# Kernel optimization log

Measured on AMD Instinct MI355X. Metric: run time of the kernel, lower is better.

Reference implementation:

```python
import jax, jax.numpy as jnp
import numpy as np
import math

N_EMBD = 1024
N_HEADS = 16
B, T = 4, 2048

def setup_inputs() -> dict:
    key = jax.random.key(0)
    k1, k2, k3 = jax.random.split(key, 3)
    x = jax.random.normal(k1, (B, T, N_EMBD), dtype=jnp.float32)
    scale = 1.0 / math.sqrt(N_EMBD)
    W_attn = jax.random.normal(k2, (N_EMBD, 3 * N_EMBD), dtype=jnp.float32) * scale
    W_proj = jax.random.normal(k3, (N_EMBD, N_EMBD), dtype=jnp.float32) * scale
    return {"x": x, "W_attn": W_attn, "W_proj": W_proj}

def reference(x, W_attn, W_proj):
    Bb, Tt, C = x.shape
    hd = C // N_HEADS
    qkv = x @ W_attn  # [B,T,3C]
    q, k, v = jnp.split(qkv, 3, axis=-1)
    # [B,H,T,hd]
    q = q.reshape(Bb, Tt, N_HEADS, hd).transpose(0, 2, 1, 3)
    k = k.reshape(Bb, Tt, N_HEADS, hd).transpose(0, 2, 1, 3)
    v = v.reshape(Bb, Tt, N_HEADS, hd).transpose(0, 2, 1, 3)
    att = jnp.einsum('bhqd,bhkd->bhqk', q, k) * (1.0 / math.sqrt(hd))
    mask = jnp.tril(jnp.ones((Tt, Tt), dtype=bool))
    att = jnp.where(mask[None, None], att, -jnp.inf)
    att = jax.nn.softmax(att, axis=-1)
    out = jnp.einsum('bhqk,bhkd->bhqd', att, v)
    out = out.transpose(0, 2, 1, 3).reshape(Bb, Tt, C)
    return out @ W_proj
```

## Files before the change

kernel.cpp:

```cpp
#include <hip/hip_runtime.h>
#include <cstddef>
#include <cstdint>

typedef __attribute__((ext_vector_type(8))) _Float16 half8;
typedef __attribute__((ext_vector_type(4))) _Float16 half4;
typedef __attribute__((ext_vector_type(4))) float f32x4;
typedef __attribute__((ext_vector_type(16))) float f32x16;

#define N_EMBD 1024
#define N_HEADS 16
#define BATCH 4
#define SEQ 2048
#define C3 3072
#define HD 64

__device__ inline uint32_t pk2(float x, float y) {
    auto h2 = __builtin_amdgcn_cvt_pkrtz(x, y);
    uint32_t u;
    __builtin_memcpy(&u, &h2, 4);
    return u;
}

__device__ inline void swap32(uint32_t& a, uint32_t& b) {
    asm volatile("v_permlane32_swap_b32 %0, %1" : "+v"(a), "+v"(b));
}

__device__ inline float exp2_hw(float x) {
    float r;
    asm("v_exp_f32 %0, %1" : "=v"(r) : "v"(x));
    return r;
}

__global__ void cvt_f32_f16(const float* __restrict__ in, _Float16* __restrict__ out, int n) {
    int i = (blockIdx.x * 256 + threadIdx.x) * 4;
    if (i >= n) return;
    float4 v = *(const float4*)(in + i);
    half4 h;
    h[0] = (_Float16)v.x; h[1] = (_Float16)v.y; h[2] = (_Float16)v.z; h[3] = (_Float16)v.w;
    *(half4*)(out + i) = h;
}

__global__ void transpose_cvt(const float* __restrict__ in, _Float16* __restrict__ out,
                              int R, int Ncols) {
    __shared__ float tile[32][33];
    int n0 = blockIdx.x * 32, r0 = blockIdx.y * 32;
    int tx = threadIdx.x, ty = threadIdx.y;
#pragma unroll
    for (int i = 0; i < 32; i += 8)
        tile[ty + i][tx] = in[(size_t)(r0 + ty + i) * Ncols + n0 + tx];
    __syncthreads();
#pragma unroll
    for (int i = 0; i < 32; i += 8)
        out[(size_t)(n0 + ty + i) * R + r0 + tx] = (_Float16)tile[tx][ty + i];
}

__global__ void transpose_v(const _Float16* __restrict__ qkv, _Float16* __restrict__ vT) {
    __shared__ _Float16 tile[32][36];
    int t0 = blockIdx.x * 32;
    int bhd = blockIdx.y;
    int bh = bhd >> 1, dh = bhd & 1;
    int b = bh >> 4, h = bh & 15;
    int tx = threadIdx.x, ty = threadIdx.y;
#pragma unroll
    for (int i = 0; i < 32; i += 8)
        tile[ty + i][tx] = qkv[(size_t)(b * SEQ + t0 + ty + i) * C3 + 2 * N_EMBD + h * HD + dh * 32 + tx];
    __syncthreads();
#pragma unroll
    for (int i = 0; i < 32; i += 8)
        vT[((size_t)bh * HD + dh * 32 + ty + i) * SEQ + t0 + tx] = tile[tx][ty + i];
}

__device__ inline void store1(float* p, float v) { *p = v; }
__device__ inline void store1(_Float16* p, float v) { *p = (_Float16)v; }

template <typename OutT>
__global__ __launch_bounds__(512, 1) void gemm192(
    const _Float16* __restrict__ A, const _Float16* __restrict__ Bt,
    OutT* __restrict__ C, int M, int N, int K) {
    __shared__ _Float16 Al[2][256 * 64];
    __shared__ _Float16 Bl[2][192 * 64];
    const int tid = threadIdx.x;
    const int lane = tid & 63, wave = tid >> 6;
    const int l15 = lane & 15, l4 = lane >> 4;
    const int wm = wave >> 2, wn = wave & 3;

    const int nwg = gridDim.x, nbx = N / 192;
    int wg = blockIdx.x;
    if ((nwg & 7) == 0) { int cpx = nwg >> 3; wg = (wg & 7) * cpx + (wg >> 3); }
    const int row0 = (wg / nbx) * 256, col0 = (wg % nbx) * 192;
    const int TAU = K >> 6;

    const int srow = tid >> 3, su = tid & 7;
    const int usrc8 = (su ^ (srow & 7)) * 8;
    auto stageAu = [&](int unit, int ts) {
        __builtin_amdgcn_global_load_lds(
            (const __attribute__((address_space(1))) void*)(A + (size_t)(row0 + unit * 64 + srow) * K + ts * 64 + usrc8),
            (__attribute__((address_space(3))) void*)(&Al[ts & 1][unit * 64 * 64 + tid * 8]), 16, 0, 0);
    };
    auto stageBu = [&](int unit, int ts) {
        __builtin_amdgcn_global_load_lds(
            (const __attribute__((address_space(1))) void*)(Bt + (size_t)(col0 + unit * 64 + srow) * K + ts * 64 + usrc8),
            (__attribute__((address_space(3))) void*)(&Bl[ts & 1][unit * 64 * 64 + tid * 8]), 16, 0, 0);
    };
    auto stageTile = [&](int ts) {
        stageAu(0, ts); stageAu(1, ts); stageAu(2, ts); stageAu(3, ts);
        stageBu(0, ts); stageBu(1, ts); stageBu(2, ts);
    };

    f32x4 acc[8][3] = {};
    stageTile(0); stageTile(1);
    asm volatile("s_waitcnt vmcnt(7)" ::: "memory");
    __builtin_amdgcn_s_barrier();

    half8 a[4][2], b[3][2];
    for (int tau = 0; tau < TAU; ++tau) {
        const _Float16* Ab = &Al[tau & 1][0];
        const _Float16* Bb = &Bl[tau & 1][0];
        const bool t2 = (tau + 2 < TAU);

#pragma unroll
        for (int m = 0; m < 4; ++m)
#pragma unroll
            for (int ks = 0; ks < 2; ++ks) {
                int r = wm * 128 + m * 16 + l15;
                a[m][ks] = *(const half8*)(Ab + r * 64 + (((ks * 4 + l4) ^ (r & 7)) * 8));
            }
#pragma unroll
        for (int n = 0; n < 3; ++n)
#pragma unroll
            for (int ks = 0; ks < 2; ++ks) {
                int r = wn * 48 + n * 16 + l15;
                b[n][ks] = *(const half8*)(Bb + r * 64 + (((ks * 4 + l4) ^ (r & 7)) * 8));
            }
        __builtin_amdgcn_s_barrier();
        __builtin_amdgcn_s_setprio(1);
#pragma unroll
        for (int m = 0; m < 4; ++m)
#pragma unroll
            for (int n = 0; n < 2; ++n)
#pragma unroll
                for (int ks = 0; ks < 2; ++ks)
                    acc[m][n] = __builtin_amdgcn_mfma_f32_16x16x32_f16(a[m][ks], b[n][ks], acc[m][n], 0, 0, 0);
        __builtin_amdgcn_s_setprio(0);
        __builtin_amdgcn_s_barrier();

        if (t2) { stageBu(0, tau + 2); stageBu(1, tau + 2); stageBu(2, tau + 2); }
        __builtin_amdgcn_s_barrier();
        __builtin_amdgcn_s_setprio(1);
#pragma unroll
        for (int m = 0; m < 4; ++m)
#pragma unroll
            for (int ks = 0; ks < 2; ++ks)
                acc[m][2] = __builtin_amdgcn_mfma_f32_16x16x32_f16(a[m][ks], b[2][ks], acc[m][2], 0, 0, 0);
        __builtin_amdgcn_s_setprio(0);
        __builtin_amdgcn_s_barrier();

#pragma unroll
        for (int m = 0; m < 4; ++m)
#pragma unroll
            for (int ks = 0; ks < 2; ++ks) {
                int r = wm * 128 + 64 + m * 16 + l15;
                a[m][ks] = *(const half8*)(Ab + r * 64 + (((ks * 4 + l4) ^ (r & 7)) * 8));
            }
        if (t2) { stageAu(0, tau + 2); stageAu(2, tau + 2); }
        __builtin_amdgcn_s_barrier();
        __builtin_amdgcn_s_setprio(1);
#pragma unroll
        for (int m = 0; m < 4; ++m)
#pragma unroll
            for (int n = 0; n < 2; ++n)
#pragma unroll
                for (int ks = 0; ks < 2; ++ks)
                    acc[4 + m][n] = __builtin_amdgcn_mfma_f32_16x16x32_f16(a[m][ks], b[n][ks], acc[4 + m][n], 0, 0, 0);
        __builtin_amdgcn_s_setprio(0);
        __builtin_amdgcn_s_barrier();

        if (t2) { stageAu(1, tau + 2); stageAu(3, tau + 2); }
        __builtin_amdgcn_s_barrier();
        __builtin_amdgcn_s_setprio(1);
#pragma unroll
        for (int m = 0; m < 4; ++m)
#pragma unroll
            for (int ks = 0; ks < 2; ++ks)
                acc[4 + m][2] = __builtin_amdgcn_mfma_f32_16x16x32_f16(a[m][ks], b[2][ks], acc[4 + m][2], 0, 0, 0);
        __builtin_amdgcn_s_setprio(0);
        if (tau <= TAU - 3) {
            asm volatile("s_waitcnt vmcnt(7)" ::: "memory");
        } else if (tau == TAU - 2) {
            asm volatile("s_waitcnt vmcnt(0)" ::: "memory");
        }
        __builtin_amdgcn_s_barrier();
    }

#pragma unroll
    for (int mi = 0; mi < 8; ++mi)
#pragma unroll
        for (int ni = 0; ni < 3; ++ni)
#pragma unroll
            for (int j = 0; j < 4; ++j) {
                int r = row0 + wm * 128 + (mi >> 2) * 64 + (mi & 3) * 16 + l4 * 4 + j;
                int c = col0 + wn * 48 + ni * 16 + l15;
                store1(C + (size_t)r * N + c, acc[mi][ni][j]);
            }
}

template <typename OutT>
__global__ __launch_bounds__(256, 2) void gemm_h(
    const _Float16* __restrict__ A, const _Float16* __restrict__ Bt,
    OutT* __restrict__ C, int M, int N, int K) {
    __shared__ _Float16 Al[128 * 32];
    __shared__ _Float16 Bl[128 * 32];
    const int tid = threadIdx.x;
    const int wave = tid >> 6, lane = tid & 63;
    const int l15 = lane & 15, l4 = lane >> 4;
    const int gx = gridDim.x;
    int lin = blockIdx.y * gx + blockIdx.x;
    int bcol, brow;
    if ((gx & 7) == 0) {
        int cpx = gx >> 3;
        int xcd = lin & 7;
        int idx = lin >> 3;
        bcol = xcd * cpx + idx % cpx;
        brow = idx / cpx;
    } else { bcol = blockIdx.x; brow = blockIdx.y; }
    const int row0 = brow * 128, col0 = bcol * 128;
    const int wm = wave >> 1, wn = wave & 1;
    f32x4 acc[4][4] = {};
    for (int k0 = 0; k0 < K; k0 += 32) {
#pragma unroll
        for (int i = 0; i < 2; ++i) {
            int c = tid + 256 * i;
            int r = c >> 2, c8 = (c & 3) * 8;
            __builtin_amdgcn_global_load_lds(
                (const __attribute__((address_space(1))) void*)(A + (size_t)(row0 + r) * K + k0 + c8),
                (__attribute__((address_space(3))) void*)(Al + (size_t)(wave * 64 + 256 * i) * 8),
                16, 0, 0);
        }
#pragma unroll
        for (int i = 0; i < 2; ++i) {
            int c = tid + 256 * i;
            int r = c >> 2, c8 = (c & 3) * 8;
            __builtin_amdgcn_global_load_lds(
                (const __attribute__((address_space(1))) void*)(Bt + (size_t)(col0 + r) * K + k0 + c8),
                (__attribute__((address_space(3))) void*)(Bl + (size_t)(wave * 64 + 256 * i) * 8),
                16, 0, 0);
        }
        __syncthreads();
        half8 a[4], b[4];
#pragma unroll
        for (int m = 0; m < 4; ++m)
            a[m] = *(const half8*)(Al + (wm * 64 + m * 16 + l15) * 32 + l4 * 8);
#pragma unroll
        for (int n = 0; n < 4; ++n)
            b[n] = *(const half8*)(Bl + (wn * 64 + n * 16 + l15) * 32 + l4 * 8);
        __builtin_amdgcn_s_setprio(1);
#pragma unroll
        for (int m = 0; m < 4; ++m)
#pragma unroll
            for (int n = 0; n < 4; ++n)
                acc[m][n] = __builtin_amdgcn_mfma_f32_16x16x32_f16(a[m], b[n], acc[m][n], 0, 0, 0);
        __builtin_amdgcn_s_setprio(0);
        __syncthreads();
    }
#pragma unroll
    for (int m = 0; m < 4; ++m)
#pragma unroll
        for (int n = 0; n < 4; ++n)
#pragma unroll
            for (int j = 0; j < 4; ++j) {
                int r = row0 + wm * 64 + m * 16 + l4 * 4 + j;
                int cc = col0 + wn * 64 + n * 16 + l15;
                store1(C + (size_t)r * N + cc, acc[m][n][j]);
            }
}

__global__ __launch_bounds__(256, 3) void attn_kernel(const _Float16* __restrict__ qkv,
                                                      const _Float16* __restrict__ vT,
                                                      _Float16* __restrict__ ao) {
    const int bid = blockIdx.x;
    const int pairp = bid >> 6;
    const int bh = bid & 63;
    const int b = bh >> 4, h = bh & 15;
    const int tid = threadIdx.x, lane = tid & 63;
    const int wave = tid >> 6;
    const int l31 = lane & 31, L = lane >> 5;

    __shared__ _Float16 Kl[3][64 * 64];
    __shared__ _Float16 Vl[3][64 * 64];

    const float qscale = 0.125f * 1.44269504089f;
    const float NEGC = -4.0f * 1.44269504089f;

    auto stage = [&](int t, int buf) {
#pragma unroll
        for (int i = 0; i < 2; ++i) {
            int idx = tid + 256 * i;
            int key = idx >> 3;
            int d8 = ((idx & 7) ^ (key & 7)) * 8;
            __builtin_amdgcn_global_load_lds(
                (const __attribute__((address_space(1))) void*)(qkv + (size_t)(b * SEQ + t * 64 + key) * C3 + N_EMBD + h * HD + d8),
                (__attribute__((address_space(3))) void*)(&Kl[buf][idx * 8]), 16, 0, 0);
        }
#pragma unroll
        for (int i = 0; i < 2; ++i) {
            int idx = tid + 256 * i;
            int d = idx >> 3;
            int k8 = ((idx & 7) ^ (d & 7)) * 8;
            __builtin_amdgcn_global_load_lds(
                (const __attribute__((address_space(1))) void*)(vT + ((size_t)bh * HD + d) * SEQ + t * 64 + k8),
                (__attribute__((address_space(3))) void*)(&Vl[buf][idx * 8]), 16, 0, 0);
        }
    };

    half8 onesf;
#pragma unroll
    for (int e = 0; e < 8; ++e) onesf[e] = (_Float16)1.0f;
    const f32x16 cinit = (f32x16)(NEGC);

    for (int pass = 0; pass < 2; ++pass) {
        const int qt = pass ? (15 - pairp) : pairp;
        const int q0w = qt * 128 + wave * 32;
        const int q_g = q0w + l31;
        const int nt = 2 * qt + 2;

        stage(0, 0);
        stage(1, 1);

        half8 qb[4];
#pragma unroll
        for (int ks = 0; ks < 4; ++ks) {
            half8 v = *(const half8*)(qkv + (size_t)(b * SEQ + q_g) * C3 + h * HD + ks * 16 + L * 8);
#pragma unroll
            for (int e = 0; e < 8; ++e) v[e] = (_Float16)((float)v[e] * qscale);
            qb[ks] = v;
        }

        f32x16 o[2];
        o[0] = (f32x16)(0.f);
        o[1] = (f32x16)(0.f);
        f32x16 lac = (f32x16)(0.f);

        asm volatile("s_waitcnt vmcnt(4)" ::: "memory");
        __builtin_amdgcn_s_barrier();

        int cur = 0;
        for (int t = 0; t < nt; ++t) {
            const int kv0 = t * 64;
            int sb = cur + 2; if (sb >= 3) sb -= 3;
            if (t + 2 < nt) stage(t + 2, sb);

            if (kv0 <= q0w + 31) {
                const _Float16* Kb = &Kl[cur][0];
                const _Float16* Vb = &Vl[cur][0];
                f32x16 s[2];
                __builtin_amdgcn_s_setprio(1);
#pragma unroll
                for (int kb = 0; kb < 2; ++kb) {
                    const int key = kb * 32 + l31;
                    {
                        half8 kf = *(const half8*)(Kb + key * 64 + ((L ^ (key & 7)) * 8));
                        s[kb] = __builtin_amdgcn_mfma_f32_32x32x16_f16(kf, qb[0], cinit, 0, 0, 0);
                    }
#pragma unroll
                    for (int ks = 1; ks < 4; ++ks) {
                        half8 kf = *(const half8*)(Kb + key * 64 + (((ks * 2 + L) ^ (key & 7)) * 8));
                        s[kb] = __builtin_amdgcn_mfma_f32_32x32x16_f16(kf, qb[ks], s[kb], 0, 0, 0);
                    }
                }
                __builtin_amdgcn_s_setprio(0);
                const bool needmask = (kv0 + 63 > q0w);
#pragma unroll
                for (int kb = 0; kb < 2; ++kb) {
#pragma unroll
                    for (int r = 0; r < 16; ++r) {
                        float v = exp2_hw(s[kb][r]);
                        if (needmask) {
                            int key_g = kv0 + kb * 32 + (r & 3) + 8 * (r >> 2) + 4 * L;
                            v = (key_g > q_g) ? 0.f : v;
                        }
                        s[kb][r] = v;
                    }
                }
                half8 paf[4];
#pragma unroll
                for (int kb = 0; kb < 2; ++kb)
#pragma unroll
                    for (int hf = 0; hf < 2; ++hf) {
                        const int bse = hf * 8;
                        uint32_t a0 = pk2(s[kb][bse + 0], s[kb][bse + 1]);
                        uint32_t b0 = pk2(s[kb][bse + 4], s[kb][bse + 5]);
                        swap32(a0, b0);
                        uint32_t a1 = pk2(s[kb][bse + 2], s[kb][bse + 3]);
                        uint32_t b1 = pk2(s[kb][bse + 6], s[kb][bse + 7]);
                        swap32(a1, b1);
                        uint32_t w[4] = {a0, a1, b0, b1};
                        __builtin_memcpy(&paf[kb * 2 + hf], w, 16);
                    }
                __builtin_amdgcn_s_setprio(1);
#pragma unroll
                for (int ks = 0; ks < 4; ++ks) {
                    lac = __builtin_amdgcn_mfma_f32_32x32x16_f16(paf[ks], onesf, lac, 0, 0, 0);
#pragma unroll
                    for (int db = 0; db < 2; ++db) {
                        const int d = db * 32 + l31;
                        half8 vb = *(const half8*)(Vb + d * 64 + (((ks * 2 + L) ^ (d & 7)) * 8));
                        o[db] = __builtin_amdgcn_mfma_f32_32x32x16_f16(paf[ks], vb, o[db], 0, 0, 0);
                    }
                }
                __builtin_amdgcn_s_setprio(0);
            }

            if (t + 2 < nt) {
                asm volatile("s_waitcnt vmcnt(4)" ::: "memory");
            } else if (t + 1 < nt) {
                asm volatile("s_waitcnt vmcnt(0)" ::: "memory");
            }
            __builtin_amdgcn_s_barrier();
            ++cur; if (cur == 3) cur = 0;
        }

#pragma unroll
        for (int db = 0; db < 2; ++db)
#pragma unroll
            for (int r = 0; r < 16; ++r) {
                int qg = q0w + (r & 3) + 8 * (r >> 2) + 4 * L;
                ao[(size_t)(b * SEQ + qg) * N_EMBD + h * HD + db * 32 + l31] =
                    (_Float16)(o[db][r] / lac[r]);
            }
    }
}

extern "C" void kernel_launch(void* const* d_in, const int* in_sizes, int n_in,
                              void* d_out, int out_size, void* d_ws, size_t ws_size,
                              hipStream_t stream) {
    const float* x  = (const float*)d_in[0];
    const float* Wa = (const float*)d_in[1];
    const float* Wp = (const float*)d_in[2];
    float* out = (float*)d_out;

    const int M = BATCH * SEQ;
    _Float16* xh  = (_Float16*)d_ws;
    _Float16* WaT = xh + (size_t)M * N_EMBD;
    _Float16* WpT = WaT + (size_t)C3 * N_EMBD;
    _Float16* qkv = WpT + (size_t)N_EMBD * N_EMBD;
    _Float16* ao  = qkv + (size_t)M * C3;
    _Float16* vT  = xh;

    int nx = M * N_EMBD;
    cvt_f32_f16<<<nx / 4 / 256, 256, 0, stream>>>(x, xh, nx);
    dim3 tb(32, 8);
    transpose_cvt<<<dim3(C3 / 32, N_EMBD / 32), tb, 0, stream>>>(Wa, WaT, N_EMBD, C3);
    transpose_cvt<<<dim3(N_EMBD / 32, N_EMBD / 32), tb, 0, stream>>>(Wp, WpT, N_EMBD, N_EMBD);

    gemm192<_Float16><<<dim3((M / 256) * (C3 / 192)), 512, 0, stream>>>(xh, WaT, qkv, M, C3, N_EMBD);

    transpose_v<<<dim3(SEQ / 32, BATCH * N_HEADS * 2), tb, 0, stream>>>(qkv, vT);

    attn_kernel<<<dim3(512), 256, 0, stream>>>(qkv, vT, ao);

    gemm_h<float><<<dim3(N_EMBD / 128, M / 128), 256, 0, stream>>>(ao, WpT, out, M, N_EMBD, N_EMBD);
}
```

Measured before the change: 187.5 us.

## Merge prep kernels into one launch and triple-buffer output projection GEMM

Folds the x conversion and both weight transpose-conversions into a single prep kernel, cutting two kernel launches. The output projection GEMM now uses three LDS buffers with direct global-to-LDS loads issued two stages ahead, waiting on vmcnt instead of a full sync. This lets loads overlap the MFMA work and halves the barriers per k-step. In exchange it triples LDS use, which may affect occupancy, and relies on hand-counted vmcnt values.

```diff
diff --git a/kernel.cpp b/kernel.cpp
--- a/kernel.cpp
+++ b/kernel.cpp
@@ -31,20 +31,10 @@
     return r;
 }
 
-__global__ void cvt_f32_f16(const float* __restrict__ in, _Float16* __restrict__ out, int n) {
-    int i = (blockIdx.x * 256 + threadIdx.x) * 4;
-    if (i >= n) return;
-    float4 v = *(const float4*)(in + i);
-    half4 h;
-    h[0] = (_Float16)v.x; h[1] = (_Float16)v.y; h[2] = (_Float16)v.z; h[3] = (_Float16)v.w;
-    *(half4*)(out + i) = h;
-}
-
-__global__ void transpose_cvt(const float* __restrict__ in, _Float16* __restrict__ out,
-                              int R, int Ncols) {
+__device__ inline void transpose_tile(const float* __restrict__ in, _Float16* __restrict__ out,
+                                      int R, int Ncols, int bx, int by, int tx, int ty) {
     __shared__ float tile[32][33];
-    int n0 = blockIdx.x * 32, r0 = blockIdx.y * 32;
-    int tx = threadIdx.x, ty = threadIdx.y;
+    int n0 = bx * 32, r0 = by * 32;
 #pragma unroll
     for (int i = 0; i < 32; i += 8)
         tile[ty + i][tx] = in[(size_t)(r0 + ty + i) * Ncols + n0 + tx];
@@ -52,6 +42,26 @@
 #pragma unroll
     for (int i = 0; i < 32; i += 8)
         out[(size_t)(n0 + ty + i) * R + r0 + tx] = (_Float16)tile[tx][ty + i];
+}
+
+__global__ void prep_kernel(const float* __restrict__ x, _Float16* __restrict__ xh,
+                            const float* __restrict__ Wa, _Float16* __restrict__ WaT,
+                            const float* __restrict__ Wp, _Float16* __restrict__ WpT) {
+    const int bid = blockIdx.x;
+    const int tx = threadIdx.x & 31, ty = threadIdx.x >> 5;
+    if (bid < 8192) {
+        int i = (bid * 256 + threadIdx.x) * 4;
+        float4 v = *(const float4*)(x + i);
+        half4 h;
+        h[0] = (_Float16)v.x; h[1] = (_Float16)v.y; h[2] = (_Float16)v.z; h[3] = (_Float16)v.w;
+        *(half4*)(xh + i) = h;
+    } else if (bid < 8192 + 3072) {
+        int v = bid - 8192;
+        transpose_tile(Wa, WaT, N_EMBD, C3, v % 96, v / 96, tx, ty);
+    } else {
+        int v = bid - 8192 - 3072;
+        transpose_tile(Wp, WpT, N_EMBD, N_EMBD, v % 32, v / 32, tx, ty);
+    }
 }
 
 __global__ void transpose_v(const _Float16* __restrict__ qkv, _Float16* __restrict__ vT) {
@@ -208,8 +218,8 @@
 __global__ __launch_bounds__(256, 2) void gemm_h(
     const _Float16* __restrict__ A, const _Float16* __restrict__ Bt,
     OutT* __restrict__ C, int M, int N, int K) {
-    __shared__ _Float16 Al[128 * 32];
-    __shared__ _Float16 Bl[128 * 32];
+    __shared__ _Float16 Al[3][128 * 32];
+    __shared__ _Float16 Bl[3][128 * 32];
     const int tid = threadIdx.x;
     const int wave = tid >> 6, lane = tid & 63;
     const int l15 = lane & 15, l4 = lane >> 4;
@@ -225,15 +235,16 @@
     } else { bcol = blockIdx.x; brow = blockIdx.y; }
     const int row0 = brow * 128, col0 = bcol * 128;
     const int wm = wave >> 1, wn = wave & 1;
-    f32x4 acc[4][4] = {};
-    for (int k0 = 0; k0 < K; k0 += 32) {
+    const int TAU = K >> 5;
+
+    auto stageT = [&](int ts, int buf) {
 #pragma unroll
         for (int i = 0; i < 2; ++i) {
             int c = tid + 256 * i;
             int r = c >> 2, c8 = (c & 3) * 8;
             __builtin_amdgcn_global_load_lds(
-                (const __attribute__((address_space(1))) void*)(A + (size_t)(row0 + r) * K + k0 + c8),
-                (__attribute__((address_space(3))) void*)(Al + (size_t)(wave * 64 + 256 * i) * 8),
+                (const __attribute__((address_space(1))) void*)(A + (size_t)(row0 + r) * K + ts * 32 + c8),
+                (__attribute__((address_space(3))) void*)(&Al[buf][(size_t)(wave * 64 + 256 * i) * 8]),
                 16, 0, 0);
         }
 #pragma unroll
@@ -241,18 +252,28 @@
             int c = tid + 256 * i;
             int r = c >> 2, c8 = (c & 3) * 8;
             __builtin_amdgcn_global_load_lds(
-                (const __attribute__((address_space(1))) void*)(Bt + (size_t)(col0 + r) * K + k0 + c8),
-                (__attribute__((address_space(3))) void*)(Bl + (size_t)(wave * 64 + 256 * i) * 8),
+                (const __attribute__((address_space(1))) void*)(Bt + (size_t)(col0 + r) * K + ts * 32 + c8),
+                (__attribute__((address_space(3))) void*)(&Bl[buf][(size_t)(wave * 64 + 256 * i) * 8]),
                 16, 0, 0);
         }
-        __syncthreads();
+    };
+
+    f32x4 acc[4][4] = {};
+    stageT(0, 0); stageT(1, 1);
+    asm volatile("s_waitcnt vmcnt(4)" ::: "memory");
+    __builtin_amdgcn_s_barrier();
+
+    int cur = 0;
+    for (int t = 0; t < TAU; ++t) {
+        int sb = cur + 2; if (sb >= 3) sb -= 3;
+        if (t + 2 < TAU) stageT(t + 2, sb);
         half8 a[4], b[4];
 #pragma unroll
         for (int m = 0; m < 4; ++m)
-            a[m] = *(const half8*)(Al + (wm * 64 + m * 16 + l15) * 32 + l4 * 8);
+            a[m] = *(const half8*)(&Al[cur][(wm * 64 + m * 16 + l15) * 32 + l4 * 8]);
 #pragma unroll
         for (int n = 0; n < 4; ++n)
-            b[n] = *(const half8*)(Bl + (wn * 64 + n * 16 + l15) * 32 + l4 * 8);
+            b[n] = *(const half8*)(&Bl[cur][(wn * 64 + n * 16 + l15) * 32 + l4 * 8]);
         __builtin_amdgcn_s_setprio(1);
 #pragma unroll
         for (int m = 0; m < 4; ++m)
@@ -260,7 +281,13 @@
             for (int n = 0; n < 4; ++n)
                 acc[m][n] = __builtin_amdgcn_mfma_f32_16x16x32_f16(a[m], b[n], acc[m][n], 0, 0, 0);
         __builtin_amdgcn_s_setprio(0);
-        __syncthreads();
+        if (t + 2 < TAU) {
+            asm volatile("s_waitcnt vmcnt(4)" ::: "memory");
+        } else if (t + 1 < TAU) {
+            asm volatile("s_waitcnt vmcnt(0)" ::: "memory");
+        }
+        __builtin_amdgcn_s_barrier();
+        ++cur; if (cur == 3) cur = 0;
     }
 #pragma unroll
     for (int m = 0; m < 4; ++m)
@@ -446,14 +473,11 @@
     _Float16* ao  = qkv + (size_t)M * C3;
     _Float16* vT  = xh;
 
-    int nx = M * N_EMBD;
-    cvt_f32_f16<<<nx / 4 / 256, 256, 0, stream>>>(x, xh, nx);
+    prep_kernel<<<dim3(8192 + 3072 + 1024), 256, 0, stream>>>(x, xh, Wa, WaT, Wp, WpT);
+
+    gemm192<_Float16><<<dim3((M / 256) * (C3 / 192)), 512, 0, stream>>>(xh, WaT, qkv, M, C3, N_EMBD);
+
     dim3 tb(32, 8);
-    transpose_cvt<<<dim3(C3 / 32, N_EMBD / 32), tb, 0, stream>>>(Wa, WaT, N_EMBD, C3);
-    transpose_cvt<<<dim3(N_EMBD / 32, N_EMBD / 32), tb, 0, stream>>>(Wp, WpT, N_EMBD, N_EMBD);
-
-    gemm192<_Float16><<<dim3((M / 256) * (C3 / 192)), 512, 0, stream>>>(xh, WaT, qkv, M, C3, N_EMBD);
-
     transpose_v<<<dim3(SEQ / 32, BATCH * N_HEADS * 2), tb, 0, stream>>>(qkv, vT);
 
     attn_kernel<<<dim3(512), 256, 0, stream>>>(qkv, vT, ao);
```

Measured after the change: 184.9 us. No clear change (-1.4%).
